# Optimization experiments

Measured on AMD Instinct MI355X. Metric: run time of the kernel, lower is better.

The kernel has to match this reference:

```python
import jax, jax.numpy as jnp
import numpy as np

B, S, R, H = 32, 512, 49, 768


def setup_inputs() -> dict:
    key = jax.random.key(0)
    ks = jax.random.split(key, 32)
    rn = lambda i, shape, s=1.0: jax.random.normal(ks[i], shape, dtype=jnp.float32) * s
    W = 0.05  # weight init scale to keep tanh/softmax in a sane range
    return {
        'text_features': rn(0, (B, S, H)),
        'img_features': rn(1, (B, R, H)),
        't1_w': rn(2, (H, H), W), 't1_b': rn(3, (H,), W),
        'i1_w': rn(4, (H, H), W),
        'a1_w': rn(5, (2 * H,), W), 'a1_b': rn(6, (), W),
        't2_w': rn(7, (H, H), W),
        'i2_w': rn(8, (H, H), W), 'i2_b': rn(9, (H,), W),
        'a2_w': rn(10, (2 * H,), W), 'a2_b': rn(11, (), W),
        'gt_w': rn(12, (H, H), W), 'gt_b': rn(13, (H,), W),
        'gi_w': rn(14, (H, H), W), 'gi_b': rn(15, (H,), W),
        'gg_w': rn(16, (2 * H, 1), W), 'gg_b': rn(17, (1,), W),
        'ft_w': rn(18, (H, H), W),
        'fm_w': rn(19, (H, H), W), 'fm_b': rn(20, (H,), W),
        'fg_w': rn(21, (2 * H, 1), W), 'fg_b': rn(22, (1,), W),
        'fr_w': rn(23, (H, H), W), 'fr_b': rn(24, (H,), W),
    }


def reference(text_features, img_features, t1_w, t1_b, i1_w, a1_w, a1_b,
              t2_w, i2_w, i2_b, a2_w, a2_b, gt_w, gt_b, gi_w, gi_b,
              gg_w, gg_b, ft_w, fm_w, fm_b, fg_w, fg_b, fr_w, fr_b):
    H = text_features.shape[-1]
    # --- CoAttention, stage 1 (text attends over image regions) ---
    # tanh(concat) is elementwise and att_linear_1 is rank-1, so split the score:
    # score[b,s,r] = tanh(t1(x_s)) . a1[:H] + tanh(i1(y_r)) . a1[H:] + b
    t_sc = jnp.tanh(text_features @ t1_w + t1_b) @ a1_w[:H]          # (B,S)
    i_sc = jnp.tanh(img_features @ i1_w) @ a1_w[H:]                  # (B,R)
    visual_att = jax.nn.softmax(t_sc[:, :, None] + i_sc[:, None, :] + a1_b, axis=-1)  # (B,S,R)
    att_img = jnp.einsum('bsr,brh->bsh', visual_att, img_features)   # (B,S,H)
    # --- CoAttention, stage 2 (attended-image queries attend over text) ---
    # concat order is [img, text] -> a2[:H] pairs with img part
    q_sc = jnp.tanh(att_img @ i2_w + i2_b) @ a2_w[:H]                # (B,S)
    k_sc = jnp.tanh(text_features @ t2_w) @ a2_w[H:]                 # (B,S)
    textual_att = jax.nn.softmax(q_sc[:, :, None] + k_sc[:, None, :] + a2_b, axis=-1)  # (B,S,S)
    att_text = jnp.einsum('bij,bjh->bih', textual_att, text_features)  # (B,S,H)
    # --- GMF gated fusion ---
    new_img = jnp.tanh(att_img @ gi_w + gi_b)
    new_txt = jnp.tanh(att_text @ gt_w + gt_b)
    gate = jax.nn.sigmoid(jnp.concatenate([new_img, new_txt], axis=-1) @ gg_w + gg_b)  # (B,S,1)
    multimodal = gate * new_img + (1.0 - gate) * new_txt
    # --- filtration gate ---
    concat_feat = jnp.concatenate([text_features @ ft_w, multimodal @ fm_w + fm_b], axis=-1)
    fgate = jax.nn.sigmoid(concat_feat @ fg_w + fg_b)                # (B,S,1)
    return fgate * jnp.tanh(multimodal @ fr_w + fr_b)
```

## Files before the change

kernel.cpp:

```cpp
#include <hip/hip_runtime.h>
#include <hip/hip_bf16.h>
#include <math.h>

constexpr int BD = 32;
constexpr int SD = 512;
constexpr int RD = 49;
constexpr int HD = 768;
constexpr int MT = BD * SD;
constexpr int MI = BD * RD;
constexpr int NP = 12;
constexpr int MBT = MT / 128;
constexpr int MBI = 13;

typedef __bf16 bf16;
typedef __bf16 bf16x4 __attribute__((ext_vector_type(4)));
typedef __bf16 bf16x8 __attribute__((ext_vector_type(8)));
typedef float f32x4 __attribute__((ext_vector_type(4)));

#define GLOAD_LDS16(g, l) __builtin_amdgcn_global_load_lds( \
    (__attribute__((address_space(1))) void*)(g),           \
    (__attribute__((address_space(3))) void*)(l), 16, 0, 0)

__device__ __forceinline__ float fast_tanh(float x) {
    const float e = __expf(2.f * x);
    return 1.f - 2.f / (e + 1.f);
}

__global__ __launch_bounds__(256) void prep_text(
    const float* __restrict__ text, const float* __restrict__ v_f,
    bf16* __restrict__ text_bf, float* __restrict__ s_txt)
{
    const int row = blockIdx.x * 4 + (threadIdx.x >> 6);
    const int lane = threadIdx.x & 63;
    const float* tr = text + (size_t)row * HD;
    bf16* tb = text_bf + (size_t)row * HD;
    float acc = 0.f;
    #pragma unroll
    for (int c = 0; c < 3; ++c) {
        const int o = c * 256 + lane * 4;
        const f32x4 x = *(const f32x4*)(tr + o);
        const f32x4 v = *(const f32x4*)(v_f + o);
        bf16x4 b; b[0] = (bf16)x[0]; b[1] = (bf16)x[1]; b[2] = (bf16)x[2]; b[3] = (bf16)x[3];
        *(bf16x4*)(tb + o) = b;
        acc += x[0] * v[0] + x[1] * v[1] + x[2] * v[2] + x[3] * v[3];
    }
    for (int off = 32; off; off >>= 1) acc += __shfl_xor(acc, off);
    if (lane == 0) s_txt[row] = acc;
}

__global__ __launch_bounds__(256) void prep_misc(
    const float* __restrict__ ft_w, const float* __restrict__ fm_w,
    const float* __restrict__ fm_b, const float* __restrict__ fg_w,
    float* __restrict__ v_f, float* __restrict__ v_m, float* __restrict__ c_m,
    const float* __restrict__ img, bf16* __restrict__ img_bf,
    const float* __restrict__ t2_w, const float* __restrict__ i1_w,
    bf16* __restrict__ wt_t, bf16* __restrict__ wt_i)
{
    __shared__ float tile[64][65];
    const int bid = blockIdx.x;
    if (bid < 385) {
        const int idx = bid * 4 + (threadIdx.x >> 6);
        const int lane = threadIdx.x & 63;
        const float* row; const float* vecp; float* outp;
        if (idx < HD)            { row = ft_w + (size_t)idx * HD;        vecp = fg_w;      outp = v_f + idx; }
        else if (idx < 2 * HD)   { row = fm_w + (size_t)(idx - HD) * HD; vecp = fg_w + HD; outp = v_m + (idx - HD); }
        else if (idx == 2 * HD)  { row = fm_b;                           vecp = fg_w + HD; outp = c_m; }
        else return;
        float acc = 0.f;
        #pragma unroll
        for (int i = 0; i < HD / 64; ++i) acc += row[lane + 64 * i] * vecp[lane + 64 * i];
        for (int off = 32; off; off >>= 1) acc += __shfl_xor(acc, off);
        if (lane == 0) *outp = acc;
    } else if (bid < 385 + 588) {
        const int i = (bid - 385) * 256 + threadIdx.x;
        const int n8 = BD * RD * HD / 8;
        if (i >= n8) return;
        const size_t o = (size_t)i * 8;
        const f32x4 x0 = *(const f32x4*)(img + o);
        const f32x4 x1 = *(const f32x4*)(img + o + 4);
        bf16x8 b;
        b[0]=(bf16)x0[0]; b[1]=(bf16)x0[1]; b[2]=(bf16)x0[2]; b[3]=(bf16)x0[3];
        b[4]=(bf16)x1[0]; b[5]=(bf16)x1[1]; b[6]=(bf16)x1[2]; b[7]=(bf16)x1[3];
        *(bf16x8*)(img_bf + o) = b;
    } else {
        const int idx2 = bid - (385 + 588);
        const int z = idx2 / 144, rem = idx2 % 144;
        const int bx = rem % 12, by = rem / 12;
        const float* W = z ? i1_w : t2_w;
        bf16* Wt = z ? wt_i : wt_t;
        const int k0 = bx * 64, n0 = by * 64;
        const int t = threadIdx.x;
        const int rb = t >> 6, c = t & 63;
        #pragma unroll
        for (int i = 0; i < 16; ++i) {
            const int r = rb + i * 4;
            tile[r][c] = W[(size_t)(k0 + r) * HD + n0 + c];
        }
        __syncthreads();
        #pragma unroll
        for (int i = 0; i < 16; ++i) {
            const int r = rb + i * 4;
            Wt[(size_t)(n0 + r) * HD + k0 + c] = (bf16)tile[c][r];
        }
    }
}

__global__ __launch_bounds__(256) void gemm2(
    const bf16* __restrict__ Atext, const bf16* __restrict__ WtT,
    const float* __restrict__ vecT, float* __restrict__ partT,
    const bf16* __restrict__ Aimg, const bf16* __restrict__ WtI,
    const float* __restrict__ vecI, float* __restrict__ partI)
{
    __shared__ __align__(16) bf16 As[128 * 32];
    __shared__ __align__(16) bf16 Bs[128 * 32];

    const bool isT = blockIdx.x < MBT;
    const bf16* A   = isT ? Atext : Aimg;
    const bf16* Wt  = isT ? WtT : WtI;
    const float* vec = isT ? vecT : vecI;
    float* part     = isT ? partT : partI;
    const int m0 = (isT ? blockIdx.x : blockIdx.x - MBT) * 128;
    const int n0 = blockIdx.y * 128;

    const int t = threadIdx.x;
    const int w = t >> 6, lane = t & 63;
    const int quad = lane >> 4, l16 = lane & 15;
    const int wm2 = (w >> 1) * 64, wn2 = (w & 1) * 64;

    const int srow = lane >> 2;
    const int scol = (lane & 3) * 8;
    const bf16* Ag = A  + (size_t)(m0 + w * 32 + srow) * HD + scol;
    const bf16* Bg = Wt + (size_t)(n0 + w * 32 + srow) * HD + scol;
    bf16* Al0 = As + (w * 32) * 32;
    bf16* Al1 = As + (w * 32 + 16) * 32;
    bf16* Bl0 = Bs + (w * 32) * 32;
    bf16* Bl1 = Bs + (w * 32 + 16) * 32;

    f32x4 acc[4][4] = {};

    for (int kk = 0; kk < HD; kk += 32) {
        GLOAD_LDS16(Ag + kk, Al0);
        GLOAD_LDS16(Ag + (size_t)16 * HD + kk, Al1);
        GLOAD_LDS16(Bg + kk, Bl0);
        GLOAD_LDS16(Bg + (size_t)16 * HD + kk, Bl1);
        __syncthreads();

        bf16x8 af[4], bg[4];
        #pragma unroll
        for (int f = 0; f < 4; ++f) {
            af[f] = *(const bf16x8*)(&As[(wm2 + f * 16 + l16) * 32 + quad * 8]);
            bg[f] = *(const bf16x8*)(&Bs[(wn2 + f * 16 + l16) * 32 + quad * 8]);
        }
        #pragma unroll
        for (int fi = 0; fi < 4; ++fi)
            #pragma unroll
            for (int fj = 0; fj < 4; ++fj)
                acc[fi][fj] = __builtin_amdgcn_mfma_f32_16x16x32_bf16(af[fi], bg[fj], acc[fi][fj], 0, 0, 0);
        __syncthreads();
    }

    float vv[4];
    #pragma unroll
    for (int fj = 0; fj < 4; ++fj) vv[fj] = vec[n0 + wn2 + fj * 16 + l16];

    #pragma unroll
    for (int fi = 0; fi < 4; ++fi) {
        #pragma unroll
        for (int reg = 0; reg < 4; ++reg) {
            float p = 0.f;
            #pragma unroll
            for (int fj = 0; fj < 4; ++fj)
                p += fast_tanh(acc[fi][fj][reg]) * vv[fj];
            p += __shfl_xor(p, 1);
            p += __shfl_xor(p, 2);
            p += __shfl_xor(p, 4);
            p += __shfl_xor(p, 8);
            if (l16 == 0) {
                const int row = m0 + wm2 + fi * 16 + quad * 4 + reg;
                part[(size_t)row * NP + blockIdx.y * 2 + (w & 1)] = p;
            }
        }
    }
}

__global__ __launch_bounds__(256) void reduce2(
    const float* __restrict__ k_part, const float* __restrict__ i_part,
    float* __restrict__ k_sc, float* __restrict__ i_sc)
{
    const int m = blockIdx.x * 256 + threadIdx.x;
    if (m < MT) {
        float s = 0.f;
        #pragma unroll
        for (int j = 0; j < NP; ++j) s += k_part[(size_t)m * NP + j];
        k_sc[m] = s;
    } else {
        const int m2 = m - MT;
        if (m2 < MI) {
            float s = 0.f;
            #pragma unroll
            for (int j = 0; j < NP; ++j) s += i_part[(size_t)m2 * NP + j];
            i_sc[m2] = s;
        }
    }
}

__global__ __launch_bounds__(256) void softmax_both(float* k_sc, float* i_sc) {
    __shared__ float red[4];
    if (blockIdx.x < BD) {
        const int b = blockIdx.x, t = threadIdx.x;
        const float x0 = k_sc[b * SD + t], x1 = k_sc[b * SD + 256 + t];
        float m = fmaxf(x0, x1);
        for (int off = 32; off; off >>= 1) m = fmaxf(m, __shfl_xor(m, off));
        if ((t & 63) == 0) red[t >> 6] = m;
        __syncthreads();
        m = fmaxf(fmaxf(red[0], red[1]), fmaxf(red[2], red[3]));
        const float e0 = expf(x0 - m), e1 = expf(x1 - m);
        float s = e0 + e1;
        for (int off = 32; off; off >>= 1) s += __shfl_xor(s, off);
        __syncthreads();
        if ((t & 63) == 0) red[t >> 6] = s;
        __syncthreads();
        s = red[0] + red[1] + red[2] + red[3];
        k_sc[b * SD + t] = e0 / s;
        k_sc[b * SD + 256 + t] = e1 / s;
    } else {
        const int b = blockIdx.x - BD, l = threadIdx.x;
        if (l < 64) {
            float x = (l < RD) ? i_sc[b * RD + l] : -1e30f;
            float m = x;
            for (int off = 32; off; off >>= 1) m = fmaxf(m, __shfl_xor(m, off));
            float e = (l < RD) ? expf(x - m) : 0.f;
            float s = e;
            for (int off = 32; off; off >>= 1) s += __shfl_xor(s, off);
            if (l < RD) i_sc[b * RD + l] = e / s;
        }
    }
}

__global__ __launch_bounds__(256) void wsum_both(
    const float* __restrict__ P1, const float* __restrict__ img,
    float* __restrict__ aimg,
    const float* __restrict__ P2, const bf16* __restrict__ text_bf,
    float* __restrict__ ws_part)
{
    __shared__ float Ps[SD];
    const int bid = blockIdx.x;
    if (bid < 96) {
        const int b = bid & 31, hy = bid >> 5;
        const int h = hy * 256 + threadIdx.x;
        for (int j = threadIdx.x; j < RD; j += 256) Ps[j] = P1[b * RD + j];
        __syncthreads();
        float acc = 0.f;
        const float* Xb = img + (size_t)b * RD * HD + h;
        for (int j = 0; j < RD; ++j) acc += Ps[j] * Xb[(size_t)j * HD];
        aimg[b * HD + h] = acc;
    } else {
        const int idx = bid - 96;
        const int q = idx / 96, rem = idx % 96;
        const int b = rem & 31, hy = rem >> 5;
        const int h = hy * 256 + threadIdx.x;
        if (threadIdx.x < 128) Ps[threadIdx.x] = P2[b * SD + q * 128 + threadIdx.x];
        __syncthreads();
        float acc = 0.f;
        const bf16* Xb = text_bf + (size_t)b * SD * HD + (size_t)(q * 128) * HD + h;
        #pragma unroll 8
        for (int j = 0; j < 128; ++j) acc += Ps[j] * (float)Xb[(size_t)j * HD];
        ws_part[((size_t)(b * 4 + q)) * HD + h] = acc;
    }
}

__global__ __launch_bounds__(256) void ni_nt_kernel(
    const float* __restrict__ aimg, const float* __restrict__ ws_part,
    const float* __restrict__ gi_w, const float* __restrict__ gi_b,
    const float* __restrict__ gt_w, const float* __restrict__ gt_b,
    float* __restrict__ ni, float* __restrict__ nt)
{
    const int b = blockIdx.x, n0 = blockIdx.y * 64, which = blockIdx.z;
    const float* W = which ? gt_w : gi_w;
    const float* bias = which ? gt_b : gi_b;
    float* Y = which ? nt : ni;

    __shared__ float Xs[HD];
    __shared__ float partial[4][64];
    const int t = threadIdx.x;
    if (which) {
        for (int h = t; h < HD; h += 256)
            Xs[h] = ws_part[((size_t)(b * 4 + 0)) * HD + h] + ws_part[((size_t)(b * 4 + 1)) * HD + h]
                  + ws_part[((size_t)(b * 4 + 2)) * HD + h] + ws_part[((size_t)(b * 4 + 3)) * HD + h];
    } else {
        for (int h = t; h < HD; h += 256) Xs[h] = aimg[b * HD + h];
    }
    __syncthreads();
    const int n = n0 + (t & 63), kq = t >> 6;
    float acc = 0.f;
    const float* Wp = W + (size_t)(kq * 192) * HD + n;
    #pragma unroll 8
    for (int h = 0; h < 192; ++h) acc += Xs[kq * 192 + h] * Wp[(size_t)h * HD];
    partial[kq][t & 63] = acc;
    __syncthreads();
    if (t < 64) {
        const float s = partial[0][t] + partial[1][t] + partial[2][t] + partial[3][t];
        Y[b * HD + n0 + t] = tanhf(s + bias[n0 + t]);
    }
}

__global__ __launch_bounds__(256) void gate_mix(
    const float* __restrict__ ni, const float* __restrict__ nt,
    const float* __restrict__ gg_w, const float* __restrict__ gg_b,
    const float* __restrict__ v_m, const float* __restrict__ c_m,
    const float* __restrict__ fg_b,
    float* __restrict__ mm, float* __restrict__ s_mm)
{
    const int b = blockIdx.x, t = threadIdx.x;
    __shared__ float red[4];
    __shared__ float gsh;
    float acc = 0.f;
    for (int n = t; n < HD; n += 256)
        acc += ni[b * HD + n] * gg_w[n] + nt[b * HD + n] * gg_w[HD + n];
    for (int off = 32; off; off >>= 1) acc += __shfl_xor(acc, off);
    if ((t & 63) == 0) red[t >> 6] = acc;
    __syncthreads();
    if (t == 0) gsh = 1.f / (1.f + expf(-(red[0] + red[1] + red[2] + red[3] + gg_b[0])));
    __syncthreads();
    const float g = gsh;
    float a2 = 0.f;
    for (int n = t; n < HD; n += 256) {
        const float m = g * ni[b * HD + n] + (1.f - g) * nt[b * HD + n];
        mm[b * HD + n] = m;
        a2 += m * v_m[n];
    }
    for (int off = 32; off; off >>= 1) a2 += __shfl_xor(a2, off);
    __syncthreads();
    if ((t & 63) == 0) red[t >> 6] = a2;
    __syncthreads();
    if (t == 0) s_mm[b] = red[0] + red[1] + red[2] + red[3] + *c_m + fg_b[0];
}

__global__ __launch_bounds__(256) void T_kernel(
    const float* __restrict__ mm, const float* __restrict__ fr_w,
    const float* __restrict__ fr_b, float* __restrict__ T)
{
    const int b = blockIdx.x, n0 = blockIdx.y * 64;
    __shared__ float Xs[HD];
    __shared__ float partial[4][64];
    const int t = threadIdx.x;
    for (int h = t; h < HD; h += 256) Xs[h] = mm[b * HD + h];
    __syncthreads();
    const int n = n0 + (t & 63), kq = t >> 6;
    float acc = 0.f;
    const float* Wp = fr_w + (size_t)(kq * 192) * HD + n;
    #pragma unroll 8
    for (int h = 0; h < 192; ++h) acc += Xs[kq * 192 + h] * Wp[(size_t)h * HD];
    partial[kq][t & 63] = acc;
    __syncthreads();
    if (t < 64) {
        const float s = partial[0][t] + partial[1][t] + partial[2][t] + partial[3][t];
        T[b * HD + n0 + t] = tanhf(s + fr_b[n0 + t]);
    }
}

__global__ __launch_bounds__(256) void out_kernel(const float* __restrict__ s_txt,
                                                  const float* __restrict__ s_mm,
                                                  const float* __restrict__ T,
                                                  float* __restrict__ out) {
    const size_t idx = ((size_t)blockIdx.x * 256 + threadIdx.x) * 4;
    const int h = (int)(idx % HD);
    const int bs = (int)(idx / HD);
    const int b = bs >> 9;
    float f = s_txt[bs] + s_mm[b];
    f = 1.f / (1.f + expf(-f));
    const float* Tp = T + b * HD + h;
    f32x4 o;
    o[0] = f * Tp[0]; o[1] = f * Tp[1]; o[2] = f * Tp[2]; o[3] = f * Tp[3];
    *(f32x4*)(out + idx) = o;
}

extern "C" void kernel_launch(void* const* d_in, const int* in_sizes, int n_in,
                              void* d_out, int out_size, void* d_ws, size_t ws_size,
                              hipStream_t stream) {
    const float* text = (const float*)d_in[0];
    const float* img  = (const float*)d_in[1];
    const float* i1_w = (const float*)d_in[4];
    const float* a1_w = (const float*)d_in[5];
    const float* t2_w = (const float*)d_in[7];
    const float* a2_w = (const float*)d_in[10];
    const float* gt_w = (const float*)d_in[12];
    const float* gt_b = (const float*)d_in[13];
    const float* gi_w = (const float*)d_in[14];
    const float* gi_b = (const float*)d_in[15];
    const float* gg_w = (const float*)d_in[16];
    const float* gg_b = (const float*)d_in[17];
    const float* ft_w = (const float*)d_in[18];
    const float* fm_w = (const float*)d_in[19];
    const float* fm_b = (const float*)d_in[20];
    const float* fg_w = (const float*)d_in[21];
    const float* fg_b = (const float*)d_in[22];
    const float* fr_w = (const float*)d_in[23];
    const float* fr_b = (const float*)d_in[24];
    float* out = (float*)d_out;

    float* sc_ = out;
    float* i_part  = sc_;
    float* k_part  = sc_ + 38400;
    float* i_sc    = sc_ + 431616;
    float* k_sc    = sc_ + 433216;
    float* aimg    = sc_ + 449600;
    float* v_f     = sc_ + 498752;
    float* v_m     = sc_ + 499520;
    float* c_m     = sc_ + 500288;
    float* ws_part = sc_ + 500352;
    float* ni      = sc_ + 598656;
    float* nt      = sc_ + 623232;
    float* mm      = sc_ + 647808;
    bf16* text_bf  = (bf16*)(sc_ + 672384);
    bf16* img_bf   = (bf16*)(sc_ + 6963840);
    bf16* wt_t     = (bf16*)(sc_ + 7565952);
    bf16* wt_i     = (bf16*)(sc_ + 7860864);

    float* ws    = (float*)d_ws;
    float* s_txt = ws;
    float* s_mm  = ws + 16384;
    float* T     = ws + 16448;

    prep_misc<<<dim3(385 + 588 + 288), dim3(256), 0, stream>>>(
        ft_w, fm_w, fm_b, fg_w, v_f, v_m, c_m, img, img_bf, t2_w, i1_w, wt_t, wt_i);
    prep_text<<<dim3(MT / 4), dim3(256), 0, stream>>>(text, v_f, text_bf, s_txt);
    gemm2<<<dim3(MBT + MBI, 6), dim3(256), 0, stream>>>(
        text_bf, wt_t, a2_w + HD, k_part, img_bf, wt_i, a1_w + HD, i_part);
    reduce2<<<dim3(MT / 256 + (MI + 255) / 256), dim3(256), 0, stream>>>(
        k_part, i_part, k_sc, i_sc);
    softmax_both<<<dim3(2 * BD), dim3(256), 0, stream>>>(k_sc, i_sc);
    wsum_both<<<dim3(96 + 384), dim3(256), 0, stream>>>(
        i_sc, img, aimg, k_sc, text_bf, ws_part);
    ni_nt_kernel<<<dim3(BD, HD / 64, 2), dim3(256), 0, stream>>>(
        aimg, ws_part, gi_w, gi_b, gt_w, gt_b, ni, nt);
    gate_mix<<<dim3(BD), dim3(256), 0, stream>>>(
        ni, nt, gg_w, gg_b, v_m, c_m, fg_b, mm, s_mm);
    T_kernel<<<dim3(BD, HD / 64), dim3(256), 0, stream>>>(mm, fr_w, fr_b, T);
    out_kernel<<<dim3((MT * HD / 4) / 256), dim3(256), 0, stream>>>(s_txt, s_mm, T, out);
}
```

Baseline: 267.1 us.

## Triple-buffer gemm2 loads, remap workgroups per XCD, fuse reduce into softmax

The gemm2 main loop moves from a single LDS buffer with two full syncs per k-step to a three-stage global_load_lds ring with explicit vmcnt waits and barriers, so loads for later k-tiles overlap the MFMA work. The LDS layout changes so each 16-row fragment is contiguous per lane. The grid is flattened and remapped so consecutive tiles land on the same XCD, which should improve L2 reuse. The separate reduce2 kernel is folded into the softmax kernel, which removes one launch and one round trip through global memory, at the cost of more LDS use and hand-tuned wait counts.

After: 275.1 us. 1.03x slower.

```diff
diff --git a/kernel.cpp b/kernel.cpp
--- a/kernel.cpp
+++ b/kernel.cpp
@@ -11,6 +11,8 @@
 constexpr int NP = 12;
 constexpr int MBT = MT / 128;
 constexpr int MBI = 13;
+constexpr int NWG = (MBT + MBI) * 6;
+constexpr int NT = HD / 32;
 
 typedef __bf16 bf16;
 typedef __bf16 bf16x4 __attribute__((ext_vector_type(4)));
@@ -20,6 +22,9 @@
 #define GLOAD_LDS16(g, l) __builtin_amdgcn_global_load_lds( \
     (__attribute__((address_space(1))) void*)(g),           \
     (__attribute__((address_space(3))) void*)(l), 16, 0, 0)
+#define BAR() __builtin_amdgcn_s_barrier()
+#define SCHED_FENCE() __builtin_amdgcn_sched_barrier(0)
+#define WAITV(n) asm volatile("s_waitcnt vmcnt(" #n ")" ::: "memory")
 
 __device__ __forceinline__ float fast_tanh(float x) {
     const float e = __expf(2.f * x);
@@ -111,53 +116,84 @@
     const bf16* __restrict__ Aimg, const bf16* __restrict__ WtI,
     const float* __restrict__ vecI, float* __restrict__ partI)
 {
-    __shared__ __align__(16) bf16 As[128 * 32];
-    __shared__ __align__(16) bf16 Bs[128 * 32];
-
-    const bool isT = blockIdx.x < MBT;
-    const bf16* A   = isT ? Atext : Aimg;
-    const bf16* Wt  = isT ? WtT : WtI;
+    __shared__ __align__(16) bf16 As[3 * 4096];
+    __shared__ __align__(16) bf16 Bs[3 * 4096];
+
+    const int bid = blockIdx.x;
+    const int q = NWG / 8, r = NWG % 8;
+    const int xcd = bid % 8, idx = bid / 8;
+    const int o = (xcd < r ? xcd * (q + 1) : r * (q + 1) + (xcd - r) * q) + idx;
+    const int mb = o / 6, nb = o % 6;
+
+    const bool isT = mb < MBT;
+    const bf16* A    = isT ? Atext : Aimg;
+    const bf16* Wt   = isT ? WtT : WtI;
     const float* vec = isT ? vecT : vecI;
-    float* part     = isT ? partT : partI;
-    const int m0 = (isT ? blockIdx.x : blockIdx.x - MBT) * 128;
-    const int n0 = blockIdx.y * 128;
+    float* part      = isT ? partT : partI;
+    const int m0 = (isT ? mb : mb - MBT) * 128;
+    const int n0 = nb * 128;
 
     const int t = threadIdx.x;
     const int w = t >> 6, lane = t & 63;
     const int quad = lane >> 4, l16 = lane & 15;
     const int wm2 = (w >> 1) * 64, wn2 = (w & 1) * 64;
 
-    const int srow = lane >> 2;
-    const int scol = (lane & 3) * 8;
-    const bf16* Ag = A  + (size_t)(m0 + w * 32 + srow) * HD + scol;
-    const bf16* Bg = Wt + (size_t)(n0 + w * 32 + srow) * HD + scol;
-    bf16* Al0 = As + (w * 32) * 32;
-    bf16* Al1 = As + (w * 32 + 16) * 32;
-    bf16* Bl0 = Bs + (w * 32) * 32;
-    bf16* Bl1 = Bs + (w * 32 + 16) * 32;
+    const bf16* Ag = A  + (size_t)(m0 + w * 32 + l16) * HD + quad * 8;
+    const bf16* Bg = Wt + (size_t)(n0 + w * 32 + l16) * HD + quad * 8;
 
     f32x4 acc[4][4] = {};
 
-    for (int kk = 0; kk < HD; kk += 32) {
-        GLOAD_LDS16(Ag + kk, Al0);
-        GLOAD_LDS16(Ag + (size_t)16 * HD + kk, Al1);
-        GLOAD_LDS16(Bg + kk, Bl0);
-        GLOAD_LDS16(Bg + (size_t)16 * HD + kk, Bl1);
-        __syncthreads();
-
-        bf16x8 af[4], bg[4];
-        #pragma unroll
-        for (int f = 0; f < 4; ++f) {
-            af[f] = *(const bf16x8*)(&As[(wm2 + f * 16 + l16) * 32 + quad * 8]);
-            bg[f] = *(const bf16x8*)(&Bs[(wn2 + f * 16 + l16) * 32 + quad * 8]);
-        }
-        #pragma unroll
-        for (int fi = 0; fi < 4; ++fi)
-            #pragma unroll
-            for (int fj = 0; fj < 4; ++fj)
-                acc[fi][fj] = __builtin_amdgcn_mfma_f32_16x16x32_bf16(af[fi], bg[fj], acc[fi][fj], 0, 0, 0);
-        __syncthreads();
-    }
+#define STAGE(tt, ss) {                                       \
+    const int ko = (tt) * 32;                                 \
+    bf16* a0 = As + (ss) * 4096 + (2 * w) * 512;              \
+    bf16* b0 = Bs + (ss) * 4096 + (2 * w) * 512;              \
+    GLOAD_LDS16(Ag + ko, a0);                                 \
+    GLOAD_LDS16(Ag + (size_t)16 * HD + ko, a0 + 512);         \
+    GLOAD_LDS16(Bg + ko, b0);                                 \
+    GLOAD_LDS16(Bg + (size_t)16 * HD + ko, b0 + 512);         \
+}
+
+#define COMPUTE(ss) {                                                   \
+    const bf16* Asl = As + (ss) * 4096;                                 \
+    const bf16* Bsl = Bs + (ss) * 4096;                                 \
+    bf16x8 af[4], bg4[4];                                               \
+    _Pragma("unroll")                                                   \
+    for (int f = 0; f < 4; ++f) {                                       \
+        af[f]  = *(const bf16x8*)(Asl + (wm2 / 16 + f) * 512 + lane * 8); \
+        bg4[f] = *(const bf16x8*)(Bsl + (wn2 / 16 + f) * 512 + lane * 8); \
+    }                                                                   \
+    _Pragma("unroll")                                                   \
+    for (int fi = 0; fi < 4; ++fi)                                      \
+        _Pragma("unroll")                                               \
+        for (int fj = 0; fj < 4; ++fj)                                  \
+            acc[fi][fj] = __builtin_amdgcn_mfma_f32_16x16x32_bf16(af[fi], bg4[fj], acc[fi][fj], 0, 0, 0); \
+}
+
+    STAGE(0, 0);
+    STAGE(1, 1);
+
+    for (int tt = 0; tt < NT - 2; ++tt) {
+        const int s2 = (tt + 2) % 3;
+        STAGE(tt + 2, s2);
+        WAITV(8);
+        BAR();
+        SCHED_FENCE();
+        COMPUTE(tt % 3);
+        SCHED_FENCE();
+        BAR();
+    }
+    WAITV(4);
+    BAR();
+    SCHED_FENCE();
+    COMPUTE((NT - 2) % 3);
+    SCHED_FENCE();
+    WAITV(0);
+    BAR();
+    SCHED_FENCE();
+    COMPUTE((NT - 1) % 3);
+
+#undef STAGE
+#undef COMPUTE
 
     float vv[4];
     #pragma unroll
@@ -177,38 +213,29 @@
             p += __shfl_xor(p, 8);
             if (l16 == 0) {
                 const int row = m0 + wm2 + fi * 16 + quad * 4 + reg;
-                part[(size_t)row * NP + blockIdx.y * 2 + (w & 1)] = p;
+                part[(size_t)row * NP + nb * 2 + (w & 1)] = p;
             }
         }
     }
 }
 
-__global__ __launch_bounds__(256) void reduce2(
+__global__ __launch_bounds__(256) void red_soft(
     const float* __restrict__ k_part, const float* __restrict__ i_part,
     float* __restrict__ k_sc, float* __restrict__ i_sc)
 {
-    const int m = blockIdx.x * 256 + threadIdx.x;
-    if (m < MT) {
-        float s = 0.f;
-        #pragma unroll
-        for (int j = 0; j < NP; ++j) s += k_part[(size_t)m * NP + j];
-        k_sc[m] = s;
-    } else {
-        const int m2 = m - MT;
-        if (m2 < MI) {
-            float s = 0.f;
-            #pragma unroll
-            for (int j = 0; j < NP; ++j) s += i_part[(size_t)m2 * NP + j];
-            i_sc[m2] = s;
-        }
-    }
-}
-
-__global__ __launch_bounds__(256) void softmax_both(float* k_sc, float* i_sc) {
     __shared__ float red[4];
     if (blockIdx.x < BD) {
         const int b = blockIdx.x, t = threadIdx.x;
-        const float x0 = k_sc[b * SD + t], x1 = k_sc[b * SD + 256 + t];
+        const float* p0 = k_part + ((size_t)b * SD + t) * NP;
+        const float* p1 = k_part + ((size_t)b * SD + 256 + t) * NP;
+        float x0 = 0.f, x1 = 0.f;
+        #pragma unroll
+        for (int j = 0; j < 3; ++j) {
+            const f32x4 a = *(const f32x4*)(p0 + j * 4);
+            const f32x4 c = *(const f32x4*)(p1 + j * 4);
+            x0 += a[0] + a[1] + a[2] + a[3];
+            x1 += c[0] + c[1] + c[2] + c[3];
+        }
         float m = fmaxf(x0, x1);
         for (int off = 32; off; off >>= 1) m = fmaxf(m, __shfl_xor(m, off));
         if ((t & 63) == 0) red[t >> 6] = m;
@@ -226,7 +253,17 @@
     } else {
         const int b = blockIdx.x - BD, l = threadIdx.x;
         if (l < 64) {
-            float x = (l < RD) ? i_sc[b * RD + l] : -1e30f;
+            float x = -1e30f;
+            if (l < RD) {
+                const float* p = i_part + ((size_t)(b * RD + l)) * NP;
+                float s0 = 0.f;
+                #pragma unroll
+                for (int j = 0; j < 3; ++j) {
+                    const f32x4 a = *(const f32x4*)(p + j * 4);
+                    s0 += a[0] + a[1] + a[2] + a[3];
+                }
+                x = s0;
+            }
             float m = x;
             for (int off = 32; off; off >>= 1) m = fmaxf(m, __shfl_xor(m, off));
             float e = (l < RD) ? expf(x - m) : 0.f;
@@ -425,11 +462,9 @@
     prep_misc<<<dim3(385 + 588 + 288), dim3(256), 0, stream>>>(
         ft_w, fm_w, fm_b, fg_w, v_f, v_m, c_m, img, img_bf, t2_w, i1_w, wt_t, wt_i);
     prep_text<<<dim3(MT / 4), dim3(256), 0, stream>>>(text, v_f, text_bf, s_txt);
-    gemm2<<<dim3(MBT + MBI, 6), dim3(256), 0, stream>>>(
+    gemm2<<<dim3(NWG), dim3(256), 0, stream>>>(
         text_bf, wt_t, a2_w + HD, k_part, img_bf, wt_i, a1_w + HD, i_part);
-    reduce2<<<dim3(MT / 256 + (MI + 255) / 256), dim3(256), 0, stream>>>(
-        k_part, i_part, k_sc, i_sc);
-    softmax_both<<<dim3(2 * BD), dim3(256), 0, stream>>>(k_sc, i_sc);
+    red_soft<<<dim3(2 * BD), dim3(256), 0, stream>>>(k_part, i_part, k_sc, i_sc);
     wsum_both<<<dim3(96 + 384), dim3(256), 0, stream>>>(
         i_sc, img, aimg, k_sc, text_bf, ws_part);
     ni_nt_kernel<<<dim3(BD, HD / 64, 2), dim3(256), 0, stream>>>(
```
